# Kernel optimization log

Hardware: AMD Instinct MI355X
Metric: run time of the kernel (lower is better)

Reference implementation:

```python
import jax, jax.numpy as jnp
import numpy as np

# Hyperparameters from module __init__
U_TH = 1.0      # firing threshold
BETA = 0.5      # membrane decay
BATCH_SIZE = 128
DELTA = 0.05    # ZO smoothing radius


def setup_inputs() -> dict:
    key = jax.random.key(0)
    k1, k2 = jax.random.split(key)
    T, B, F = 32, BATCH_SIZE, 8192
    inputs = jax.random.normal(k1, (T * B, F), dtype=jnp.float32)
    # 'sample once' Gaussian ZO tangents, same shape as inputs
    random_tangents = jax.random.normal(k2, (T * B, F), dtype=jnp.float32)
    return {"inputs": inputs, "random_tangents": random_tangents}


def reference(inputs, random_tangents):
    """Leaky integrate-and-fire over time with LocalZO (single-sample)
    surrogate gradient. inputs: [T*B, F] with T = leading//BATCH_SIZE."""
    orig_shape = inputs.shape
    T = inputs.shape[0] // BATCH_SIZE
    x = inputs.reshape(T, BATCH_SIZE, *inputs.shape[1:])
    z = random_tangents.reshape(T, BATCH_SIZE, *inputs.shape[1:])

    def step(u, xt_zt):
        xt, zt = xt_zt
        u = BETA * u + xt                      # membrane update
        v = u - U_TH                           # distance to threshold
        # LocalZO single-sample surrogate: |z|/(2*delta) * 1(|v| < delta*|z|)
        surr = jax.lax.stop_gradient(
            (jnp.abs(zt) / (2.0 * DELTA))
            * (jnp.abs(v) < DELTA * jnp.abs(zt)).astype(xt.dtype)
        )
        h = (v > 0).astype(xt.dtype)           # hard spike
        # straight-through: forward = h, d spike / d v = surr
        spike = jax.lax.stop_gradient(h - surr * v) + surr * v
        u = u - spike * U_TH                   # soft reset (subtract threshold)
        return u, spike

    u0 = jnp.zeros_like(x[0])
    _, spikes = jax.lax.scan(step, u0, (x, z))
    return spikes.reshape(orig_shape)
```

## Files before the change

kernel.cpp:

```cpp
#include <hip/hip_runtime.h>


constexpr int BATCH = 128;
constexpr int FDIM  = 8192;
constexpr int STEP  = BATCH * FDIM;
constexpr int VEC   = 2;

typedef float f32x2 __attribute__((ext_vector_type(2)));

__device__ __forceinline__ float lif_step(float& u, float xs, float zs)
{
    float uu = 0.5f * u;
    uu = uu + xs;
    float v = uu - 1.0f;
    float az   = fabsf(zs);
    float ind  = (fabsf(v) < 0.05f * az) ? 1.0f : 0.0f;
    float surr = (az / 0.1f) * ind;
    float h    = (v > 0.0f) ? 1.0f : 0.0f;
    float a     = surr * v;
    float spike = (h - a) + a;
    u = uu - spike * 1.0f;
    return spike;
}

__global__ __launch_bounds__(256) void lif_zo_kernel(
    const float* __restrict__ x,
    const float* __restrict__ z,
    float* __restrict__ out,
    int T)
{
#pragma clang fp contract(off)
    const int tid = blockIdx.x * blockDim.x + threadIdx.x;
    long idx = (long)tid * VEC;

    float u0 = 0.0f, u1 = 0.0f;

    f32x2 xt = *reinterpret_cast<const f32x2*>(x + idx);
    f32x2 zt = *reinterpret_cast<const f32x2*>(z + idx);

    for (int t = 0; t < T; ++t) {
        const long nidx = idx + ((t + 1 < T) ? (long)STEP : 0);
        f32x2 xn = *reinterpret_cast<const f32x2*>(x + nidx);
        f32x2 zn = *reinterpret_cast<const f32x2*>(z + nidx);

        f32x2 s;
        s.x = lif_step(u0, xt.x, zt.x);
        s.y = lif_step(u1, xt.y, zt.y);

        __builtin_nontemporal_store(s, reinterpret_cast<f32x2*>(out + idx));

        idx = idx + STEP;
        xt = xn;
        zt = zn;
    }
}

extern "C" void kernel_launch(void* const* d_in, const int* in_sizes, int n_in,
                              void* d_out, int out_size, void* d_ws, size_t ws_size,
                              hipStream_t stream)
{
    const float* x = (const float*)d_in[0];
    const float* z = (const float*)d_in[1];
    float* out = (float*)d_out;

    const int total = in_sizes[0];
    const int T = total / STEP;

    const int nthreads = STEP / VEC;
    const int block = 256;
    const int grid = nthreads / block;

    lif_zo_kernel<<<grid, block, 0, stream>>>(x, z, out, T);
}
```

Baseline: 322.4 us.

## Widen to float4 per thread and prefetch three timesteps ahead

```diff
diff --git a/kernel.cpp b/kernel.cpp
--- a/kernel.cpp
+++ b/kernel.cpp
@@ -4,12 +4,11 @@
 constexpr int BATCH = 128;
 constexpr int FDIM  = 8192;
 constexpr int STEP  = BATCH * FDIM;
-constexpr int VEC   = 2;
-
-typedef float f32x2 __attribute__((ext_vector_type(2)));
+constexpr int VEC   = 4;
 
 __device__ __forceinline__ float lif_step(float& u, float xs, float zs)
 {
+#pragma clang fp contract(off)
     float uu = 0.5f * u;
     uu = uu + xs;
     float v = uu - 1.0f;
@@ -31,27 +30,37 @@
 {
 #pragma clang fp contract(off)
     const int tid = blockIdx.x * blockDim.x + threadIdx.x;
-    long idx = (long)tid * VEC;
+    const long base = (long)tid * VEC;
 
-    float u0 = 0.0f, u1 = 0.0f;
+    float u[VEC] = {0.0f, 0.0f, 0.0f, 0.0f};
+    float4 xb[4], zb[4];
 
-    f32x2 xt = *reinterpret_cast<const f32x2*>(x + idx);
-    f32x2 zt = *reinterpret_cast<const f32x2*>(z + idx);
+#pragma unroll
+    for (int k = 0; k < 3; ++k) {
+        const int tk = (k < T) ? k : (T - 1);
+        const long a = base + (long)tk * STEP;
+        xb[k] = *reinterpret_cast<const float4*>(x + a);
+        zb[k] = *reinterpret_cast<const float4*>(z + a);
+    }
 
+    long widx = base;
+#pragma unroll 4
     for (int t = 0; t < T; ++t) {
-        const long nidx = idx + ((t + 1 < T) ? (long)STEP : 0);
-        f32x2 xn = *reinterpret_cast<const f32x2*>(x + nidx);
-        f32x2 zn = *reinterpret_cast<const f32x2*>(z + nidx);
+        long p = widx + 3L * (long)STEP;
+        if (t + 3 >= T) p = widx;
+        xb[(t + 3) & 3] = *reinterpret_cast<const float4*>(x + p);
+        zb[(t + 3) & 3] = *reinterpret_cast<const float4*>(z + p);
 
-        f32x2 s;
-        s.x = lif_step(u0, xt.x, zt.x);
-        s.y = lif_step(u1, xt.y, zt.y);
+        const float4 xt = xb[t & 3];
+        const float4 zt = zb[t & 3];
+        float4 s;
+        s.x = lif_step(u[0], xt.x, zt.x);
+        s.y = lif_step(u[1], xt.y, zt.y);
+        s.z = lif_step(u[2], xt.z, zt.z);
+        s.w = lif_step(u[3], xt.w, zt.w);
 
-        __builtin_nontemporal_store(s, reinterpret_cast<f32x2*>(out + idx));
-
-        idx = idx + STEP;
-        xt = xn;
-        zt = zn;
+        *reinterpret_cast<float4*>(out + widx) = s;
+        widx += STEP;
     }
 }
 
```

Measured after the change: 329.7 us. +2.3%, slower.
